# Kernel optimization log

Measured on AMD Instinct MI355X. Metric: run time of the kernel, lower is better.

## Reference

```python
import jax, jax.numpy as jnp
import numpy as np

B, S, D = 2, 2048, 1024
H = 16
DK = D // H
SCALE = 1.0 / np.sqrt(DK)

def setup_inputs() -> dict:
    key = jax.random.key(0)
    ks = jax.random.split(key, 11)
    std = 1.0 / np.sqrt(D)
    return {
        "query": jax.random.normal(ks[0], (B, S, D), jnp.float32),
        "key":   jax.random.normal(ks[1], (B, S, D), jnp.float32),
        "value": jax.random.normal(ks[2], (B, S, D), jnp.float32),
        "Wq": jax.random.normal(ks[3], (D, H * DK), jnp.float32) * std,
        "bq": jnp.zeros((H * DK,), jnp.float32),
        "Wk": jax.random.normal(ks[4], (D, H * DK), jnp.float32) * std,
        "bk": jnp.zeros((H * DK,), jnp.float32),
        "Wv": jax.random.normal(ks[5], (D, H * DK), jnp.float32) * std,
        "bv": jnp.zeros((H * DK,), jnp.float32),
        "Wo": jax.random.normal(ks[6], (D, D), jnp.float32) * std,
        "bo": jnp.zeros((D,), jnp.float32),
    }

def reference(query, key, value, Wq, bq, Wk, bk, Wv, bv, Wo, bo):
    b, s, _ = query.shape
    # projections -> [b, s, h, d_k]
    q = (query @ Wq + bq).reshape(b, s, H, DK)
    k = (key   @ Wk + bk).reshape(b, s, H, DK)
    v = (value @ Wv + bv).reshape(b, s, H, DK)
    # scores [b, i, j, h]
    scores = jnp.einsum('bihd,bjhd->bijh', q, k) * SCALE
    attn = jax.nn.softmax(scores, axis=2)  # softmax over key dim j
    # dropout rate 0.0 (eval mode) -> identity
    x = jnp.einsum('bijh,bjhd->bihd', attn, v).reshape(b, s, H * DK)
    return x @ Wo + bo
```

## Files before the change

kernel.cpp:

```cpp
#include <hip/hip_runtime.h>
#include <hip/hip_bf16.h>
#include <math.h>
#include <stdint.h>

constexpr int Bb = 2, Ss = 2048, Dd = 1024, Hh = 16;
constexpr int Mm = Bb * Ss;
constexpr int Nn = Dd;
constexpr int Kk = Dd;
constexpr float QSCALE = 0.125f * 1.44269504088896340736f;

typedef unsigned short ushort_t;
typedef __attribute__((ext_vector_type(8))) short bf16x8;
typedef __attribute__((ext_vector_type(4))) short bf16x4;
typedef __attribute__((ext_vector_type(4))) float f32x4;

#if __has_builtin(__builtin_amdgcn_exp2f)
#define EXP2F(x) __builtin_amdgcn_exp2f(x)
#else
#define EXP2F(x) exp2f(x)
#endif

__device__ __forceinline__ ushort_t f2bf(float f) {
  union { float f; unsigned u; } v; v.f = f;
  return (ushort_t)((v.u + 0x7fff + ((v.u >> 16) & 1)) >> 16);
}

__device__ __forceinline__ f32x4 mfma16(bf16x4 a, bf16x4 b, f32x4 c) {
#if __has_builtin(__builtin_amdgcn_mfma_f32_16x16x16bf16_1k)
  return __builtin_amdgcn_mfma_f32_16x16x16bf16_1k(a, b, c, 0, 0, 0);
#else
  asm("v_mfma_f32_16x16x16_bf16 %0, %1, %2, %0" : "+v"(c) : "v"(a), "v"(b));
  return c;
#endif
}

__device__ __forceinline__ void load16_lds(const void* g, void* l) {
  __builtin_amdgcn_global_load_lds(
      (const __attribute__((address_space(1))) void*)(uintptr_t)g,
      (__attribute__((address_space(3))) void*)(uint32_t)(uintptr_t)l, 16, 0, 0);
}

__global__ __launch_bounds__(256) void prep(
    const float* __restrict__ q, const float* __restrict__ k,
    const float* __restrict__ v, ushort_t* __restrict__ qkvb,
    const float* __restrict__ Wq, const float* __restrict__ Wk,
    const float* __restrict__ Wv, const float* __restrict__ Wo,
    ushort_t* __restrict__ Wt) {
  const int bid = blockIdx.x;
  const int tid = threadIdx.x;
  if (bid < 12288) {
    const int z = bid >> 12, xi = bid & 4095;
    const float* src = (z == 0) ? q : (z == 1) ? k : v;
    ushort_t* dst = qkvb + (size_t)z * Mm * Kk;
    const size_t idx = ((size_t)xi * 256 + tid) * 4;
    const float4 val = *(const float4*)(src + idx);
    ushort4 o;
    o.x = f2bf(val.x); o.y = f2bf(val.y); o.z = f2bf(val.z); o.w = f2bf(val.w);
    *(ushort4*)(dst + idx) = o;
    return;
  }
  const int bid2 = bid - 12288;
  const int z = bid2 >> 8, rem = bid2 & 255;
  const float* W = (z == 0) ? Wq : (z == 1) ? Wk : (z == 2) ? Wv : Wo;
  ushort_t* out = Wt + (size_t)z * Kk * Nn;
  __shared__ float t[64][65];
  const int n0 = (rem & 15) * 64, k0 = (rem >> 4) * 64;
  const int lr = tid >> 4, lc = (tid & 15) * 4;
#pragma unroll
  for (int i = 0; i < 4; i++) {
    const int r = lr + i * 16;
    const float4 vv = *(const float4*)(W + (size_t)(k0 + r) * Nn + n0 + lc);
    t[r][lc] = vv.x; t[r][lc + 1] = vv.y; t[r][lc + 2] = vv.z; t[r][lc + 3] = vv.w;
  }
  __syncthreads();
  const int n = tid >> 2, kc = (tid & 3) * 16;
  ushort_t tmp[16];
#pragma unroll
  for (int j = 0; j < 16; j++) tmp[j] = f2bf(t[kc + j][n]);
  ushort_t* op = out + (size_t)(n0 + n) * Kk + k0 + kc;
  ((uint4*)op)[0] = ((uint4*)tmp)[0];
  ((uint4*)op)[1] = ((uint4*)tmp)[1];
}

__global__ __launch_bounds__(256) void transpose_v(
    const ushort_t* __restrict__ Vp, ushort_t* __restrict__ Vt) {
  __shared__ ushort_t t[64][68];
  const int tid = threadIdx.x;
  const int s0 = blockIdx.x * 64, h = blockIdx.y, b = blockIdx.z;
  const int lr = tid >> 4, lc = (tid & 15) * 4;
#pragma unroll
  for (int i = 0; i < 4; i++) {
    const int r = lr + i * 16;
    const ushort4 v =
        *(const ushort4*)(Vp + (size_t)(b * Ss + s0 + r) * Dd + h * 64 + lc);
    *(ushort4*)&t[r][lc] = v;
  }
  __syncthreads();
  const int d = tid >> 2, sc = (tid & 3) * 16;
  ushort_t tmp[16];
#pragma unroll
  for (int j = 0; j < 16; j++) tmp[j] = t[sc + j][d];
  ushort_t* op = Vt + ((size_t)b * Dd + h * 64 + d) * Ss + s0 + sc;
  ((uint4*)op)[0] = ((uint4*)tmp)[0];
  ((uint4*)op)[1] = ((uint4*)tmp)[1];
}

template <int BN, bool OUT_BF16>
__global__ __launch_bounds__(256) void gemm_mfma(
    const ushort_t* __restrict__ Abase, size_t a_stride,
    const ushort_t* __restrict__ Wbase, size_t w_stride,
    const float* __restrict__ bias0, const float* __restrict__ bias1,
    const float* __restrict__ bias2, void* __restrict__ Cbase, size_t c_stride,
    float scale_z0) {
  constexpr int BM = 128, BK = 32;
  constexpr int WM = (BN == 128) ? 64 : 32;
  constexpr int MT_ = WM / 16, NT_ = 4;
  __shared__ ushort_t As[BM * BK];
  __shared__ ushort_t Bs[BN * BK];
  const int tid = threadIdx.x, lane = tid & 63, wid = tid >> 6;
  const int z = blockIdx.z;
  const ushort_t* A = Abase + (size_t)z * a_stride;
  const ushort_t* Wt = Wbase + (size_t)z * w_stride;
  const float* bias = (z == 0) ? bias0 : (z == 1) ? bias1 : bias2;
  const float sc = (z == 0) ? scale_z0 : 1.0f;
  const int m0 = blockIdx.y * BM, n0 = blockIdx.x * BN;
  const int wm = (BN == 128) ? (wid >> 1) * 64 : wid * 32;
  const int wn = (BN == 128) ? (wid & 1) * 64 : 0;
  const int quad = lane >> 4, r16 = lane & 15;
  const int srow = lane >> 2;
  const int scol = (lane & 3) * 8;

  f32x4 acc[MT_][NT_];
#pragma unroll
  for (int m = 0; m < MT_; m++)
#pragma unroll
    for (int n = 0; n < NT_; n++) acc[m][n] = f32x4{0.f, 0.f, 0.f, 0.f};

  for (int k0 = 0; k0 < Kk; k0 += BK) {
    __syncthreads();
#pragma unroll
    for (int i = 0; i < BM / 64; i++) {
      const int I = wid * (BM / 64) + i;
      load16_lds(A + (size_t)(m0 + I * 16 + srow) * Kk + k0 + scol, As + I * 512);
    }
#pragma unroll
    for (int i = 0; i < BN / 64; i++) {
      const int I = wid * (BN / 64) + i;
      load16_lds(Wt + (size_t)(n0 + I * 16 + srow) * Kk + k0 + scol, Bs + I * 512);
    }
    __syncthreads();
    bf16x8 af[MT_], bfr[NT_];
#pragma unroll
    for (int m = 0; m < MT_; m++)
      af[m] = *(const bf16x8*)(As + (wm + m * 16 + r16) * BK + quad * 8);
#pragma unroll
    for (int n = 0; n < NT_; n++)
      bfr[n] = *(const bf16x8*)(Bs + (wn + n * 16 + r16) * BK + quad * 8);
#pragma unroll
    for (int m = 0; m < MT_; m++)
#pragma unroll
      for (int n = 0; n < NT_; n++)
        acc[m][n] =
            __builtin_amdgcn_mfma_f32_16x16x32_bf16(af[m], bfr[n], acc[m][n], 0, 0, 0);
  }

#pragma unroll
  for (int m = 0; m < MT_; m++) {
#pragma unroll
    for (int n = 0; n < NT_; n++) {
      const int gc = n0 + wn + n * 16 + r16;
      const float bv = bias[gc];
#pragma unroll
      for (int r = 0; r < 4; r++) {
        const int gr = m0 + wm + m * 16 + quad * 4 + r;
        const float v = (acc[m][n][r] + bv) * sc;
        if (OUT_BF16)
          ((ushort_t*)Cbase)[(size_t)z * c_stride + (size_t)gr * Nn + gc] = f2bf(v);
        else
          ((float*)Cbase)[(size_t)z * c_stride + (size_t)gr * Nn + gc] = v;
      }
    }
  }
}

__global__ __launch_bounds__(256, 3) void flash_mfma(
    const ushort_t* __restrict__ Qp, const ushort_t* __restrict__ Kp,
    const ushort_t* __restrict__ Vt, ushort_t* __restrict__ Xp) {
  __shared__ __align__(16) char smem[2 * 64 * 68 * 4];
  ushort_t* KsU = (ushort_t*)smem;
  ushort_t* VtsU = KsU + 2 * 4096;

  const int tid = threadIdx.x, lane = tid & 63, wid = tid >> 6;
  const int lid = blockIdx.x + (blockIdx.y << 5) + (blockIdx.z << 9);
  const int swzb = ((lid & 7) << 7) + (lid >> 3);
  const int qt = swzb & 31, h = (swzb >> 5) & 15, b = swzb >> 9;
  const int quad = lane >> 4, r16 = lane & 15;
  const int row8 = lane >> 3;
  const int colsw = ((lane & 7) ^ row8) * 8;
  const int swz = r16 & 7;

  const ushort_t* Qg = Qp + ((size_t)(b * Ss + qt * 64)) * Dd + h * 64;
  const ushort_t* Kg = Kp + ((size_t)b * Ss) * Dd + h * 64;
  const ushort_t* Vg = Vt + ((size_t)b * Dd + h * 64) * Ss;

  bf16x8 qf[2][4];
#pragma unroll
  for (int n = 0; n < 4; n++)
#pragma unroll
    for (int ks = 0; ks < 2; ks++)
      qf[ks][n] = *(const bf16x8*)(Qg + (size_t)(n * 16 + r16) * Dd + ks * 32 + quad * 8);

  const uint32_t kbase = (uint32_t)(wid * 16 + r16) * 64;
  const uint32_t koff0 = kbase + (uint32_t)(((0 * 4 + quad) ^ swz) << 3);
  const uint32_t koff1 = kbase + (uint32_t)(((1 * 4 + quad) ^ swz) << 3);
  const int vG = wid * 2 + (quad >> 1);
  const uint32_t vcol = (uint32_t)(((vG ^ swz) << 3) + (quad & 1) * 4);

  f32x4 acc[4][4];
#pragma unroll
  for (int mt = 0; mt < 4; mt++)
#pragma unroll
    for (int n = 0; n < 4; n++) acc[mt][n] = f32x4{0.f, 0.f, 0.f, 0.f};
  float rsn[4] = {0.f, 0.f, 0.f, 0.f};

  auto stage = [&](int kt, int bsel) {
#pragma unroll
    for (int i = 0; i < 2; i++) {
      const int I = wid * 2 + i;
      load16_lds(Kg + (size_t)(kt * 64 + I * 8 + row8) * Dd + colsw,
                 KsU + bsel * 4096 + I * 512);
      load16_lds(Vg + (size_t)(I * 8 + row8) * Ss + kt * 64 + colsw,
                 VtsU + bsel * 4096 + I * 512);
    }
  };

  stage(0, 0);
  asm volatile("s_waitcnt vmcnt(4)" ::: "memory");

  for (int kt = 0; kt < Ss / 64; kt++) {
    const int cur = kt & 1;
    if (kt + 1 < Ss / 64) {
      stage(kt + 1, cur ^ 1);
      asm volatile("s_waitcnt vmcnt(4)\n\ts_barrier" ::: "memory");
    } else {
      asm volatile("s_waitcnt vmcnt(0)\n\ts_barrier" ::: "memory");
    }
    const ushort_t* Kc = KsU + cur * 4096;
    const ushort_t* Vc = VtsU + cur * 4096;

    const bf16x8 kf0 = *(const bf16x8*)(Kc + koff0);
    const bf16x8 kf1 = *(const bf16x8*)(Kc + koff1);
    f32x4 sacc[4];
#pragma unroll
    for (int n = 0; n < 4; n++) sacc[n] = f32x4{0.f, 0.f, 0.f, 0.f};
    __builtin_amdgcn_s_setprio(1);
#pragma unroll
    for (int n = 0; n < 4; n++)
      sacc[n] = __builtin_amdgcn_mfma_f32_16x16x32_bf16(kf0, qf[0][n], sacc[n], 0, 0, 0);
#pragma unroll
    for (int n = 0; n < 4; n++)
      sacc[n] = __builtin_amdgcn_mfma_f32_16x16x32_bf16(kf1, qf[1][n], sacc[n], 0, 0, 0);
    __builtin_amdgcn_s_setprio(0);

    bf16x4 pf[4];
#pragma unroll
    for (int n = 0; n < 4; n++) {
      const float p0 = EXP2F(sacc[n][0]), p1 = EXP2F(sacc[n][1]);
      const float p2 = EXP2F(sacc[n][2]), p3 = EXP2F(sacc[n][3]);
      rsn[n] += (p0 + p1) + (p2 + p3);
      union { __hip_bfloat162 hh; unsigned u; } lo, hi;
      lo.hh = __float22bfloat162_rn(make_float2(p0, p1));
      hi.hh = __float22bfloat162_rn(make_float2(p2, p3));
      union { uint2 u2; bf16x4 v; } pk;
      pk.u2 = make_uint2(lo.u, hi.u);
      pf[n] = pk.v;
    }

    bf16x4 vf[4];
#pragma unroll
    for (int mt = 0; mt < 4; mt++)
      vf[mt] = *(const bf16x4*)(Vc + (uint32_t)(mt * 16 + r16) * 64 + vcol);
    __builtin_amdgcn_s_setprio(1);
#pragma unroll
    for (int mt = 0; mt < 4; mt++)
#pragma unroll
      for (int n = 0; n < 4; n++)
        acc[mt][n] = mfma16(vf[mt], pf[n], acc[mt][n]);
    __builtin_amdgcn_s_setprio(0);

    asm volatile("s_barrier" ::: "memory");
  }

#pragma unroll
  for (int n = 0; n < 4; n++) {
    float r = rsn[n];
    r += __shfl_xor(r, 16, 64);
    r += __shfl_xor(r, 32, 64);
    rsn[n] = r;
  }

  float* red = (float*)smem;
  __syncthreads();
  if (wid & 2) {
    float* p = red + (size_t)(wid & 1) * (64 * 68) + (size_t)lane * 68;
#pragma unroll
    for (int mt = 0; mt < 4; mt++)
#pragma unroll
      for (int n = 0; n < 4; n++)
        *(f32x4*)(p + (mt * 4 + n) * 4) = acc[mt][n];
    p[64] = rsn[0]; p[65] = rsn[1]; p[66] = rsn[2]; p[67] = rsn[3];
  }
  __syncthreads();
  if (!(wid & 2)) {
    const float* p = red + (size_t)wid * (64 * 68) + (size_t)lane * 68;
#pragma unroll
    for (int mt = 0; mt < 4; mt++)
#pragma unroll
      for (int n = 0; n < 4; n++)
        acc[mt][n] += *(const f32x4*)(p + (mt * 4 + n) * 4);
    rsn[0] += p[64]; rsn[1] += p[65]; rsn[2] += p[66]; rsn[3] += p[67];
  }
  __syncthreads();
  if (wid == 1) {
    float* p = red + (size_t)lane * 68;
#pragma unroll
    for (int mt = 0; mt < 4; mt++)
#pragma unroll
      for (int n = 0; n < 4; n++)
        *(f32x4*)(p + (mt * 4 + n) * 4) = acc[mt][n];
    p[64] = rsn[0]; p[65] = rsn[1]; p[66] = rsn[2]; p[67] = rsn[3];
  }
  __syncthreads();
  if (wid == 0) {
    const float* p = red + (size_t)lane * 68;
#pragma unroll
    for (int mt = 0; mt < 4; mt++)
#pragma unroll
      for (int n = 0; n < 4; n++)
        acc[mt][n] += *(const f32x4*)(p + (mt * 4 + n) * 4);
    rsn[0] += p[64]; rsn[1] += p[65]; rsn[2] += p[66]; rsn[3] += p[67];
    float inv[4];
#pragma unroll
    for (int n = 0; n < 4; n++) inv[n] = 1.0f / rsn[n];
#pragma unroll
    for (int mt = 0; mt < 4; mt++) {
#pragma unroll
      for (int n = 0; n < 4; n++) {
        ushort4 o;
        o.x = f2bf(acc[mt][n][0] * inv[n]);
        o.y = f2bf(acc[mt][n][1] * inv[n]);
        o.z = f2bf(acc[mt][n][2] * inv[n]);
        o.w = f2bf(acc[mt][n][3] * inv[n]);
        *(ushort4*)(Xp + (size_t)(b * Ss + qt * 64 + n * 16 + r16) * Dd +
                    h * 64 + mt * 16 + quad * 4) = o;
      }
    }
  }
}

extern "C" void kernel_launch(void* const* d_in, const int* in_sizes, int n_in,
                              void* d_out, int out_size, void* d_ws,
                              size_t ws_size, hipStream_t stream) {
  const float* q  = (const float*)d_in[0];
  const float* k  = (const float*)d_in[1];
  const float* v  = (const float*)d_in[2];
  const float* Wq = (const float*)d_in[3];
  const float* bq = (const float*)d_in[4];
  const float* Wk = (const float*)d_in[5];
  const float* bk = (const float*)d_in[6];
  const float* Wv = (const float*)d_in[7];
  const float* bv = (const float*)d_in[8];
  const float* Wo = (const float*)d_in[9];
  const float* bo = (const float*)d_in[10];

  ushort_t* ws = (ushort_t*)d_ws;
  const size_t MD = (size_t)Mm * Kk;
  const size_t KN = (size_t)Kk * Nn;
  ushort_t* qkvb = ws;
  ushort_t* Wt   = ws + 3 * MD;
  ushort_t* QKVp = Wt + 4 * KN;
  ushort_t* Vtp  = QKVp + 3 * MD;
  ushort_t* Xp   = qkvb;

  prep<<<dim3(13312), 256, 0, stream>>>(q, k, v, qkvb, Wq, Wk, Wv, Wo, Wt);
  gemm_mfma<128, true><<<dim3(Nn / 128, Mm / 128, 3), 256, 0, stream>>>(
      qkvb, MD, Wt, KN, bq, bk, bv, QKVp, MD, QSCALE);
  transpose_v<<<dim3(Ss / 64, Hh, Bb), 256, 0, stream>>>(QKVp + 2 * MD, Vtp);
  flash_mfma<<<dim3(Ss / 64, Hh, Bb), 256, 0, stream>>>(QKVp, QKVp + MD, Vtp, Xp);
  gemm_mfma<64, false><<<dim3(Nn / 64, Mm / 128, 1), 256, 0, stream>>>(
      Xp, 0, Wt + 3 * KN, 0, bo, bo, bo, d_out, 0, 1.0f);
}
```

Before: 237.3 us.

## Load K/V fragments directly from global and merge PV into 16x16x32 MFMAs

The flash attention kernel stops staging K and V tiles through double-buffered LDS with global_load_lds and barriers. Each wave now reads its K and V fragments straight from global memory into registers, two 64-key tiles per iteration. The P*V product of the two tiles is combined into a single 16x16x32 MFMA in place of two 16x16x16 ones. This removes per-tile barriers and LDS traffic, but every wave now issues redundant uncoalesced global loads with no explicit prefetch, so latency hiding depends on occupancy and the caches.

```diff
diff --git a/kernel.cpp b/kernel.cpp
--- a/kernel.cpp
+++ b/kernel.cpp
@@ -11,7 +11,6 @@
 
 typedef unsigned short ushort_t;
 typedef __attribute__((ext_vector_type(8))) short bf16x8;
-typedef __attribute__((ext_vector_type(4))) short bf16x4;
 typedef __attribute__((ext_vector_type(4))) float f32x4;
 
 #if __has_builtin(__builtin_amdgcn_exp2f)
@@ -23,15 +22,6 @@
 __device__ __forceinline__ ushort_t f2bf(float f) {
   union { float f; unsigned u; } v; v.f = f;
   return (ushort_t)((v.u + 0x7fff + ((v.u >> 16) & 1)) >> 16);
-}
-
-__device__ __forceinline__ f32x4 mfma16(bf16x4 a, bf16x4 b, f32x4 c) {
-#if __has_builtin(__builtin_amdgcn_mfma_f32_16x16x16bf16_1k)
-  return __builtin_amdgcn_mfma_f32_16x16x16bf16_1k(a, b, c, 0, 0, 0);
-#else
-  asm("v_mfma_f32_16x16x16_bf16 %0, %1, %2, %0" : "+v"(c) : "v"(a), "v"(b));
-  return c;
-#endif
 }
 
 __device__ __forceinline__ void load16_lds(const void* g, void* l) {
@@ -186,23 +176,21 @@
 __global__ __launch_bounds__(256, 3) void flash_mfma(
     const ushort_t* __restrict__ Qp, const ushort_t* __restrict__ Kp,
     const ushort_t* __restrict__ Vt, ushort_t* __restrict__ Xp) {
-  __shared__ __align__(16) char smem[2 * 64 * 68 * 4];
-  ushort_t* KsU = (ushort_t*)smem;
-  ushort_t* VtsU = KsU + 2 * 4096;
+  __shared__ float red[2 * 64 * 68];
 
   const int tid = threadIdx.x, lane = tid & 63, wid = tid >> 6;
   const int lid = blockIdx.x + (blockIdx.y << 5) + (blockIdx.z << 9);
   const int swzb = ((lid & 7) << 7) + (lid >> 3);
   const int qt = swzb & 31, h = (swzb >> 5) & 15, b = swzb >> 9;
   const int quad = lane >> 4, r16 = lane & 15;
-  const int row8 = lane >> 3;
-  const int colsw = ((lane & 7) ^ row8) * 8;
-  const int swz = r16 & 7;
 
   const ushort_t* Qg = Qp + ((size_t)(b * Ss + qt * 64)) * Dd + h * 64;
   const ushort_t* Kg = Kp + ((size_t)b * Ss) * Dd + h * 64;
   const ushort_t* Vg = Vt + ((size_t)b * Dd + h * 64) * Ss;
 
+  const ushort_t* Kw = Kg + (size_t)(wid * 16 + r16) * Dd + quad * 8;
+  const ushort_t* Vw = Vg + (size_t)r16 * Ss + wid * 16 + quad * 4;
+
   bf16x8 qf[2][4];
 #pragma unroll
   for (int n = 0; n < 4; n++)
@@ -210,12 +198,6 @@
     for (int ks = 0; ks < 2; ks++)
       qf[ks][n] = *(const bf16x8*)(Qg + (size_t)(n * 16 + r16) * Dd + ks * 32 + quad * 8);
 
-  const uint32_t kbase = (uint32_t)(wid * 16 + r16) * 64;
-  const uint32_t koff0 = kbase + (uint32_t)(((0 * 4 + quad) ^ swz) << 3);
-  const uint32_t koff1 = kbase + (uint32_t)(((1 * 4 + quad) ^ swz) << 3);
-  const int vG = wid * 2 + (quad >> 1);
-  const uint32_t vcol = (uint32_t)(((vG ^ swz) << 3) + (quad & 1) * 4);
-
   f32x4 acc[4][4];
 #pragma unroll
   for (int mt = 0; mt < 4; mt++)
@@ -223,46 +205,33 @@
     for (int n = 0; n < 4; n++) acc[mt][n] = f32x4{0.f, 0.f, 0.f, 0.f};
   float rsn[4] = {0.f, 0.f, 0.f, 0.f};
 
-  auto stage = [&](int kt, int bsel) {
-#pragma unroll
-    for (int i = 0; i < 2; i++) {
-      const int I = wid * 2 + i;
-      load16_lds(Kg + (size_t)(kt * 64 + I * 8 + row8) * Dd + colsw,
-                 KsU + bsel * 4096 + I * 512);
-      load16_lds(Vg + (size_t)(I * 8 + row8) * Ss + kt * 64 + colsw,
-                 VtsU + bsel * 4096 + I * 512);
-    }
-  };
-
-  stage(0, 0);
-  asm volatile("s_waitcnt vmcnt(4)" ::: "memory");
-
-  for (int kt = 0; kt < Ss / 64; kt++) {
-    const int cur = kt & 1;
-    if (kt + 1 < Ss / 64) {
-      stage(kt + 1, cur ^ 1);
-      asm volatile("s_waitcnt vmcnt(4)\n\ts_barrier" ::: "memory");
-    } else {
-      asm volatile("s_waitcnt vmcnt(0)\n\ts_barrier" ::: "memory");
-    }
-    const ushort_t* Kc = KsU + cur * 4096;
-    const ushort_t* Vc = VtsU + cur * 4096;
-
-    const bf16x8 kf0 = *(const bf16x8*)(Kc + koff0);
-    const bf16x8 kf1 = *(const bf16x8*)(Kc + koff1);
+  for (int kt2 = 0; kt2 < Ss / 128; kt2++) {
+    const size_t offA = (size_t)(kt2 * 128) * Dd;
+    const size_t offB = offA + (size_t)64 * Dd;
+    const int colA = kt2 * 128, colB = colA + 64;
+
+    bf16x8 kfA0 = *(const bf16x8*)(Kw + offA);
+    bf16x8 kfA1 = *(const bf16x8*)(Kw + offA + 32);
+    bf16x8 kfB0 = *(const bf16x8*)(Kw + offB);
+    bf16x8 kfB1 = *(const bf16x8*)(Kw + offB + 32);
+    uint2 vA[4];
+#pragma unroll
+    for (int mt = 0; mt < 4; mt++)
+      vA[mt] = *(const uint2*)(Vw + (size_t)(mt * 16) * Ss + colA);
+
     f32x4 sacc[4];
 #pragma unroll
     for (int n = 0; n < 4; n++) sacc[n] = f32x4{0.f, 0.f, 0.f, 0.f};
     __builtin_amdgcn_s_setprio(1);
 #pragma unroll
     for (int n = 0; n < 4; n++)
-      sacc[n] = __builtin_amdgcn_mfma_f32_16x16x32_bf16(kf0, qf[0][n], sacc[n], 0, 0, 0);
+      sacc[n] = __builtin_amdgcn_mfma_f32_16x16x32_bf16(kfA0, qf[0][n], sacc[n], 0, 0, 0);
 #pragma unroll
     for (int n = 0; n < 4; n++)
-      sacc[n] = __builtin_amdgcn_mfma_f32_16x16x32_bf16(kf1, qf[1][n], sacc[n], 0, 0, 0);
+      sacc[n] = __builtin_amdgcn_mfma_f32_16x16x32_bf16(kfA1, qf[1][n], sacc[n], 0, 0, 0);
     __builtin_amdgcn_s_setprio(0);
 
-    bf16x4 pf[4];
+    uint2 pA[4];
 #pragma unroll
     for (int n = 0; n < 4; n++) {
       const float p0 = EXP2F(sacc[n][0]), p1 = EXP2F(sacc[n][1]);
@@ -271,24 +240,48 @@
       union { __hip_bfloat162 hh; unsigned u; } lo, hi;
       lo.hh = __float22bfloat162_rn(make_float2(p0, p1));
       hi.hh = __float22bfloat162_rn(make_float2(p2, p3));
-      union { uint2 u2; bf16x4 v; } pk;
-      pk.u2 = make_uint2(lo.u, hi.u);
+      pA[n] = make_uint2(lo.u, hi.u);
+    }
+    uint2 vB[4];
+#pragma unroll
+    for (int mt = 0; mt < 4; mt++)
+      vB[mt] = *(const uint2*)(Vw + (size_t)(mt * 16) * Ss + colB);
+
+#pragma unroll
+    for (int n = 0; n < 4; n++) sacc[n] = f32x4{0.f, 0.f, 0.f, 0.f};
+    __builtin_amdgcn_s_setprio(1);
+#pragma unroll
+    for (int n = 0; n < 4; n++)
+      sacc[n] = __builtin_amdgcn_mfma_f32_16x16x32_bf16(kfB0, qf[0][n], sacc[n], 0, 0, 0);
+#pragma unroll
+    for (int n = 0; n < 4; n++)
+      sacc[n] = __builtin_amdgcn_mfma_f32_16x16x32_bf16(kfB1, qf[1][n], sacc[n], 0, 0, 0);
+    __builtin_amdgcn_s_setprio(0);
+
+    bf16x8 pf[4];
+#pragma unroll
+    for (int n = 0; n < 4; n++) {
+      const float p0 = EXP2F(sacc[n][0]), p1 = EXP2F(sacc[n][1]);
+      const float p2 = EXP2F(sacc[n][2]), p3 = EXP2F(sacc[n][3]);
+      rsn[n] += (p0 + p1) + (p2 + p3);
+      union { __hip_bfloat162 hh; unsigned u; } lo, hi;
+      lo.hh = __float22bfloat162_rn(make_float2(p0, p1));
+      hi.hh = __float22bfloat162_rn(make_float2(p2, p3));
+      union { uint4 u; bf16x8 v; } pk;
+      pk.u = make_uint4(pA[n].x, pA[n].y, lo.u, hi.u);
       pf[n] = pk.v;
     }
 
-    bf16x4 vf[4];
-#pragma unroll
-    for (int mt = 0; mt < 4; mt++)
-      vf[mt] = *(const bf16x4*)(Vc + (uint32_t)(mt * 16 + r16) * 64 + vcol);
     __builtin_amdgcn_s_setprio(1);
 #pragma unroll
-    for (int mt = 0; mt < 4; mt++)
-#pragma unroll
-      for (int n = 0; n < 4; n++)
-        acc[mt][n] = mfma16(vf[mt], pf[n], acc[mt][n]);
+    for (int mt = 0; mt < 4; mt++) {
+      union { uint4 u; bf16x8 v; } vk;
+      vk.u = make_uint4(vA[mt].x, vA[mt].y, vB[mt].x, vB[mt].y);
+#pragma unroll
+      for (int n = 0; n < 4; n++)
+        acc[mt][n] = __builtin_amdgcn_mfma_f32_16x16x32_bf16(vk.v, pf[n], acc[mt][n], 0, 0, 0);
+    }
     __builtin_amdgcn_s_setprio(0);
-
-    asm volatile("s_barrier" ::: "memory");
   }
 
 #pragma unroll
@@ -299,7 +292,6 @@
     rsn[n] = r;
   }
 
-  float* red = (float*)smem;
   __syncthreads();
   if (wid & 2) {
     float* p = red + (size_t)(wid & 1) * (64 * 68) + (size_t)lane * 68;
```

Measured after the change: 276.3 us. 16.4% more time.
